# Kernel tuning notes

Measured on AMD Instinct MI355X. Metric: run time of the kernel, lower is better.

Reference implementation:

```python
import jax, jax.numpy as jnp
import numpy as np

INPUT_SIZE = 1024
HIDDEN_SIZE = 1024
BATCH = 8192


def setup_inputs() -> dict:
    key = jax.random.key(0)
    ks = jax.random.split(key, 10)
    H, I, B = HIDDEN_SIZE, INPUT_SIZE, BATCH
    s = 1.0 / np.sqrt(H)  # scale params so activations stay in sane range
    return {
        "input": jax.random.normal(ks[0], (B, I), jnp.float32),
        "hx": jax.random.normal(ks[1], (B, H), jnp.float32),
        "cx": jax.random.normal(ks[2], (B, H), jnp.float32),
        "att": jax.random.normal(ks[3], (B, I), jnp.float32),
        "weight_ih": jax.random.normal(ks[4], (4 * H, I), jnp.float32) * s,
        "weight_hh": jax.random.normal(ks[5], (4 * H, H), jnp.float32) * s,
        "bias_ih": jax.random.normal(ks[6], (4 * H,), jnp.float32),
        "bias_hh": jax.random.normal(ks[7], (4 * H,), jnp.float32),
        "weight_att": jax.random.normal(ks[8], (2 * H, I), jnp.float32) * s,
        "bias_att": jax.random.normal(ks[9], (2 * H,), jnp.float32),
    }


def reference(input, hx, cx, att, weight_ih, weight_hh, bias_ih, bias_hh,
              weight_att, bias_att):
    H = weight_hh.shape[1]
    # gates: [B, 4H]
    gates = input @ weight_ih.T + bias_ih + hx @ weight_hh.T + bias_hh
    att_gates = att @ weight_att.T + bias_att  # [B, 2H]
    ingate, forgetgate, cellgate, outgate = jnp.split(gates, 4, axis=1)
    ingate_att, attgate = jnp.split(att_gates, 2, axis=1)
    ingate = jax.nn.sigmoid(ingate)
    forgetgate = jax.nn.sigmoid(forgetgate)
    cellgate = jnp.tanh(cellgate)
    ingate_att = jax.nn.sigmoid(ingate_att)
    attgate = jnp.tanh(attgate)
    outgate = jax.nn.sigmoid(outgate)
    cy = forgetgate * cx + ingate * cellgate + ingate_att * attgate
    hy = outgate * jnp.tanh(cy)
    return (hy, cy)
```

## Files before the change

kernel.cpp:

```cpp
#include <hip/hip_runtime.h>


typedef __attribute__((ext_vector_type(8))) __bf16 bf16x8;
typedef __attribute__((ext_vector_type(8))) unsigned short ushort8;
typedef __attribute__((ext_vector_type(4))) float f32x4;
typedef __attribute__((ext_vector_type(2))) unsigned int u32x2;

#define AS1 __attribute__((address_space(1)))
#define AS3 __attribute__((address_space(3)))

__device__ __forceinline__ void gld16(const unsigned short* g, unsigned short* l) {
    __builtin_amdgcn_global_load_lds((const AS1 void*)g, (AS3 void*)l, 16, 0, 0);
}

__device__ __forceinline__ unsigned short f2bf(float f) {
    unsigned int u = __builtin_bit_cast(unsigned int, f);
    u += 0x7fffu + ((u >> 16) & 1u);
    return (unsigned short)(u >> 16);
}

__device__ __forceinline__ unsigned int cvtpk(float lo, float hi) {
    unsigned int r;
    asm("v_cvt_pk_bf16_f32 %0, %1, %2" : "=v"(r) : "v"(lo), "v"(hi));
    return r;
}

__device__ __forceinline__ float bf2f(unsigned short u) {
    unsigned int x = ((unsigned int)u) << 16;
    return __builtin_bit_cast(float, x);
}

__device__ __forceinline__ float sigmoidf_(float x) { return 1.f / (1.f + __expf(-x)); }
__device__ __forceinline__ float tanhf_(float x) {
    float e = __expf(-2.f * fabsf(x));
    float t = (1.f - e) / (1.f + e);
    return x >= 0.f ? t : -t;
}

__device__ __forceinline__ bf16x8 ldfrag(const unsigned short* p) {
    return __builtin_bit_cast(bf16x8, *(const ushort8*)p);
}

#define BARRIER __builtin_amdgcn_s_barrier()
#define LGKM_(n) asm volatile("s_waitcnt lgkmcnt(" #n ")" ::: "memory")
#define LGKM(n)  LGKM_(n)
#define FENCE    asm volatile("" ::: "memory")
#define VMW_(n) asm volatile("s_waitcnt vmcnt(" #n ")" ::: "memory")
#define VMW(n)  VMW_(n)
#define PRIO1   __builtin_amdgcn_s_setprio(1)
#define PRIO0   __builtin_amdgcn_s_setprio(0)
#define MFMA16(a, b, c) __builtin_amdgcn_mfma_f32_16x16x32_bf16(a, b, c, 0, 0, 0)

__global__ __launch_bounds__(256) void cast_all_k(
    const float* __restrict__ input, const float* __restrict__ hx,
    const float* __restrict__ att,   const float* __restrict__ w_ih,
    const float* __restrict__ w_hh,  const float* __restrict__ w_att,
    unsigned short* __restrict__ XH, unsigned short* __restrict__ ATTb,
    unsigned short* __restrict__ W4, unsigned short* __restrict__ WA)
{
    const int u = blockIdx.x * 256 + threadIdx.x;
    const float* src; unsigned short* dst; int ld, off, rel;
    if      (u < 2097152) { src = input; dst = XH;   ld = 2048; off = 0;    rel = u; }
    else if (u < 4194304) { src = hx;    dst = XH;   ld = 2048; off = 1024; rel = u - 2097152; }
    else if (u < 6291456) { src = att;   dst = ATTb; ld = 1024; off = 0;    rel = u - 4194304; }
    else if (u < 7340032) { src = w_ih;  dst = W4;   ld = 2048; off = 0;    rel = u - 6291456; }
    else if (u < 8388608) { src = w_hh;  dst = W4;   ld = 2048; off = 1024; rel = u - 7340032; }
    else                  { src = w_att; dst = WA;   ld = 1024; off = 0;    rel = u - 8388608; }

    const float4 v = *(const float4*)(src + rel * 4);
    u32x2 q;
    q[0] = cvtpk(v.x, v.y);
    q[1] = cvtpk(v.z, v.w);
    const int row = rel >> 8, c4 = rel & 255;
    *(u32x2*)(dst + row * ld + off + c4 * 4) = q;
}

__global__ __launch_bounds__(512, 2) void fused_gemm_k(
    const unsigned short* __restrict__ XH, const unsigned short* __restrict__ W4,
    const unsigned short* __restrict__ ATTb, const unsigned short* __restrict__ WA,
    const float* __restrict__ b_ih, const float* __restrict__ b_hh,
    const float* __restrict__ bias_att,
    const float* __restrict__ cx, unsigned short* __restrict__ attS,
    float* __restrict__ out)
{
    __shared__ unsigned short As[2][16384];
    __shared__ unsigned short Bs[2][16384];

    const int tid  = threadIdx.x;
    const int wave = tid >> 6, lane = tid & 63;
    const int l15 = lane & 15, quad = lane >> 4;
    const int wr = wave >> 2, wn = wave & 3;

    const int orig  = blockIdx.x;
    const int xcd   = orig & 7, local = orig >> 3;
    const int row0  = (xcd * 4 + (local & 3)) * 256;
    const int n0    = (local >> 2) * 64;

    const int rl = tid >> 3;
    const int c8 = (tid & 7) ^ (rl & 7);
    unsigned aG = (unsigned)(row0 + rl) * 2048u + (unsigned)c8 * 8u;
    unsigned bG = (unsigned)(((rl >> 4) & 3) * 1024 + n0 + (rl & 15)) * 2048u + (unsigned)c8 * 8u;
    unsigned aA = (unsigned)(row0 + rl) * 1024u + (unsigned)c8 * 8u;
    unsigned bA = (unsigned)(((rl >> 4) & 1) * 1024 + n0 + ((rl >> 5) & 1) * 16 + (rl & 15)) * 1024u
                  + (unsigned)c8 * 8u;

    auto stageA_att = [&](int buf) {
#pragma unroll
        for (int h = 0; h < 2; ++h)
#pragma unroll
            for (int p = 0; p < 2; ++p)
                gld16(ATTb + aA + (unsigned)(h * 131072 + p * 65536),
                      &As[buf][h * 8192 + (tid + p * 512) * 8]);
        aA += 64;
    };
    auto stageB_att = [&](int buf) {
#pragma unroll
        for (int h = 0; h < 2; ++h)
            gld16(WA + bA + (unsigned)(h * 32768), &Bs[buf][(h * 512 + tid) * 8]);
        bA += 64;
    };
    auto stageA_g = [&](int buf) {
#pragma unroll
        for (int h = 0; h < 2; ++h)
#pragma unroll
            for (int p = 0; p < 2; ++p)
                gld16(XH + aG + (unsigned)(h * 262144 + p * 131072),
                      &As[buf][h * 8192 + (tid + p * 512) * 8]);
        aG += 64;
    };
    auto stageB_g = [&](int buf) {
#pragma unroll
        for (int h = 0; h < 2; ++h)
#pragma unroll
            for (int p = 0; p < 2; ++p)
                gld16(W4 + bG + (unsigned)(h * 65536 + p * 32768),
                      &Bs[buf][h * 8192 + (tid + p * 512) * 8]);
        bG += 64;
    };

    const int swz0 = (quad ^ (l15 & 7)) * 8;
    const int swz1 = ((4 + quad) ^ (l15 & 7)) * 8;
    const int aro  = (wr * 128 + l15) * 64;
    const int brG  = (wn * 64 + l15) * 64;
    const int brA  = (wn * 32 + l15) * 64;

    const f32x4 z = {0.f, 0.f, 0.f, 0.f};
    const int col = n0 + wn * 16 + l15;

    {
        f32x4 acc2[8][2];
#pragma unroll
        for (int i = 0; i < 8; ++i) { acc2[i][0] = z; acc2[i][1] = z; }

        auto att_slice = [&](int buf, int sw) {
            bf16x8 aS[8], bS[2];
#pragma unroll
            for (int i = 0; i < 4; ++i) aS[i] = ldfrag(&As[buf][aro + i * 1024 + sw]);
#pragma unroll
            for (int j = 0; j < 2; ++j) bS[j] = ldfrag(&Bs[buf][brA + j * 1024 + sw]);
            FENCE;
#pragma unroll
            for (int i = 0; i < 4; ++i) aS[4 + i] = ldfrag(&As[buf][aro + (4 + i) * 1024 + sw]);
            BARRIER; LGKM(4);
            PRIO1;
#pragma unroll
            for (int i = 0; i < 4; ++i)
#pragma unroll
                for (int j = 0; j < 2; ++j)
                    acc2[i][j] = MFMA16(aS[i], bS[j], acc2[i][j]);
            LGKM(0);
#pragma unroll
            for (int i = 0; i < 4; ++i)
#pragma unroll
                for (int j = 0; j < 2; ++j)
                    acc2[4 + i][j] = MFMA16(aS[4 + i], bS[j], acc2[4 + i][j]);
            PRIO0;
            BARRIER;
        };

        stageA_att(0); stageB_att(0);
        for (int g = 0; g < 8; ++g) {
            stageA_att(1); stageB_att(1);
            VMW(6); BARRIER;
            att_slice(0, swz0);
            att_slice(0, swz1);
            if (g < 7) { stageA_att(0); stageB_att(0); VMW(6); }
            else       { VMW(0); }
            BARRIER;
            att_slice(1, swz0);
            att_slice(1, swz1);
        }

        const float ba0 = bias_att[col], ba1 = bias_att[1024 + col];
#pragma unroll
        for (int i = 0; i < 8; ++i) {
            const int lr = wr * 128 + i * 16 + quad * 4;
#pragma unroll
            for (int r = 0; r < 4; ++r) {
                float v = sigmoidf_(acc2[i][0][r] + ba0) * tanhf_(acc2[i][1][r] + ba1);
                attS[(unsigned)(row0 + lr + r) * 1024u + (unsigned)col] = f2bf(v);
            }
        }
    }

    f32x4 acc[8][4];
#pragma unroll
    for (int i = 0; i < 8; ++i)
#pragma unroll
        for (int j = 0; j < 4; ++j) acc[i][j] = z;

    auto gates_group = [&](int buf, bool iss) {
        bf16x8 aF0[4], aF1[4], aH0[4], aH1[4], bL0[2], bL1[2], bH0[2], bH1[2];
#pragma unroll
        for (int i = 0; i < 4; ++i) aF0[i] = ldfrag(&As[buf][aro + i * 1024 + swz0]);
#pragma unroll
        for (int j = 0; j < 2; ++j) bL0[j] = ldfrag(&Bs[buf][brG + j * 1024 + swz0]);
        FENCE;
#pragma unroll
        for (int i = 0; i < 4; ++i) aF1[i] = ldfrag(&As[buf][aro + i * 1024 + swz1]);
#pragma unroll
        for (int j = 0; j < 2; ++j) bL1[j] = ldfrag(&Bs[buf][brG + j * 1024 + swz1]);
        BARRIER; LGKM(6);
        PRIO1;
#pragma unroll
        for (int i = 0; i < 4; ++i)
#pragma unroll
            for (int j = 0; j < 2; ++j)
                acc[i][j] = MFMA16(aF0[i], bL0[j], acc[i][j]);
        LGKM(0);
#pragma unroll
        for (int i = 0; i < 4; ++i)
#pragma unroll
            for (int j = 0; j < 2; ++j)
                acc[i][j] = MFMA16(aF1[i], bL1[j], acc[i][j]);
        PRIO0;
        BARRIER;
#pragma unroll
        for (int j = 0; j < 2; ++j) bH0[j] = ldfrag(&Bs[buf][brG + (2 + j) * 1024 + swz0]);
        FENCE;
#pragma unroll
        for (int j = 0; j < 2; ++j) bH1[j] = ldfrag(&Bs[buf][brG + (2 + j) * 1024 + swz1]);
        BARRIER; LGKM(2);
        PRIO1;
#pragma unroll
        for (int i = 0; i < 4; ++i)
#pragma unroll
            for (int j = 0; j < 2; ++j)
                acc[i][2 + j] = MFMA16(aF0[i], bH0[j], acc[i][2 + j]);
        LGKM(0);
#pragma unroll
        for (int i = 0; i < 4; ++i)
#pragma unroll
            for (int j = 0; j < 2; ++j)
                acc[i][2 + j] = MFMA16(aF1[i], bH1[j], acc[i][2 + j]);
        PRIO0;
        BARRIER;
#pragma unroll
        for (int i = 0; i < 4; ++i) aH0[i] = ldfrag(&As[buf][aro + (4 + i) * 1024 + swz0]);
        FENCE;
#pragma unroll
        for (int i = 0; i < 4; ++i) aH1[i] = ldfrag(&As[buf][aro + (4 + i) * 1024 + swz1]);
        if (iss) stageB_g(buf);
        BARRIER; LGKM(4);
        PRIO1;
#pragma unroll
        for (int i = 0; i < 4; ++i)
#pragma unroll
            for (int j = 0; j < 2; ++j)
                acc[4 + i][2 + j] = MFMA16(aH0[i], bH0[j], acc[4 + i][2 + j]);
        LGKM(0);
#pragma unroll
        for (int i = 0; i < 4; ++i)
#pragma unroll
            for (int j = 0; j < 2; ++j)
                acc[4 + i][2 + j] = MFMA16(aH1[i], bH1[j], acc[4 + i][2 + j]);
        PRIO0;
        BARRIER;
        if (iss) stageA_g(buf);
        PRIO1;
#pragma unroll
        for (int i = 0; i < 4; ++i)
#pragma unroll
            for (int j = 0; j < 2; ++j) {
                acc[4 + i][j] = MFMA16(aH0[i], bL0[j], acc[4 + i][j]);
                acc[4 + i][j] = MFMA16(aH1[i], bL1[j], acc[4 + i][j]);
            }
        PRIO0;
    };

    stageA_g(0); stageB_g(0); stageA_g(1); stageB_g(1);
    VMW(8); BARRIER;
#pragma unroll 2
    for (int t = 0; t < 30; ++t) {
        gates_group(t & 1, true);
        VMW(8); BARRIER;
    }
    gates_group(0, false); VMW(0); BARRIER;
    gates_group(1, false);
    BARRIER;

    float* sF = (float*)(&As[0][0]);
    float* sC = (float*)(&Bs[0][0]);
    const float bi  = b_ih[col]        + b_hh[col];
    const float bff = b_ih[1024 + col] + b_hh[1024 + col];
    const float bg  = b_ih[2048 + col] + b_hh[2048 + col];
    const float bo  = b_ih[3072 + col] + b_hh[3072 + col];
    const int lcol  = wn * 16 + l15;
    const int CYOFF = 8192 * 1024;

#pragma unroll
    for (int i = 0; i < 8; ++i)
#pragma unroll
        for (int r = 0; r < 4; ++r) {
            const int lr = wr * 128 + i * 16 + quad * 4 + r;
            const int pc = lcol ^ (((lr >> 2) & 1) << 4);
            const float attv = bf2f(attS[(unsigned)(row0 + lr) * 1024u + (unsigned)col]);
            sF[lr * 64 + pc] = sigmoidf_(acc[i][1][r] + bff);
            sC[lr * 64 + pc] = sigmoidf_(acc[i][0][r] + bi) * tanhf_(acc[i][2][r] + bg)
                               + attv;
        }
    BARRIER;

    const int rr = tid >> 4;
    const int cc = (tid & 15) * 4;
#pragma unroll
    for (int p = 0; p < 8; ++p) {
        const int row = p * 32 + rr;
        const int pcc = cc ^ (((row >> 2) & 1) << 4);
        f32x4 fg4 = *(f32x4*)&sF[row * 64 + pcc];
        f32x4 cp4 = *(f32x4*)&sC[row * 64 + pcc];
        const float4 cx4 = *(const float4*)&cx[(row0 + row) * 1024 + n0 + cc];
        f32x4 cy4;
        cy4[0] = fg4[0] * cx4.x + cp4[0];
        cy4[1] = fg4[1] * cx4.y + cp4[1];
        cy4[2] = fg4[2] * cx4.z + cp4[2];
        cy4[3] = fg4[3] * cx4.w + cp4[3];
        *(f32x4*)&out[CYOFF + (row0 + row) * 1024 + n0 + cc] = cy4;
        *(f32x4*)&sF[row * 64 + pcc] = cy4;
    }
    BARRIER;

#pragma unroll
    for (int i = 0; i < 8; ++i)
#pragma unroll
        for (int r = 0; r < 4; ++r) {
            const int lr = wr * 128 + i * 16 + quad * 4 + r;
            const int pc = lcol ^ (((lr >> 2) & 1) << 4);
            sC[lr * 64 + pc] = sigmoidf_(acc[i][3][r] + bo);
        }
    BARRIER;

#pragma unroll
    for (int p = 0; p < 8; ++p) {
        const int row = p * 32 + rr;
        const int pcc = cc ^ (((row >> 2) & 1) << 4);
        f32x4 og4 = *(f32x4*)&sC[row * 64 + pcc];
        f32x4 cy4 = *(f32x4*)&sF[row * 64 + pcc];
        f32x4 hy4;
        hy4[0] = og4[0] * tanhf_(cy4[0]);
        hy4[1] = og4[1] * tanhf_(cy4[1]);
        hy4[2] = og4[2] * tanhf_(cy4[2]);
        hy4[3] = og4[3] * tanhf_(cy4[3]);
        *(f32x4*)&out[(row0 + row) * 1024 + n0 + cc] = hy4;
    }
}

extern "C" void kernel_launch(void* const* d_in, const int* in_sizes, int n_in,
                              void* d_out, int out_size, void* d_ws, size_t ws_size,
                              hipStream_t stream) {
    const float* input = (const float*)d_in[0];
    const float* hx    = (const float*)d_in[1];
    const float* cx    = (const float*)d_in[2];
    const float* att   = (const float*)d_in[3];
    const float* w_ih  = (const float*)d_in[4];
    const float* w_hh  = (const float*)d_in[5];
    const float* b_ih  = (const float*)d_in[6];
    const float* b_hh  = (const float*)d_in[7];
    const float* w_att = (const float*)d_in[8];
    const float* b_att = (const float*)d_in[9];
    float* out = (float*)d_out;

    char* ws = (char*)d_ws;
    unsigned short* XH   = (unsigned short*)(ws);
    unsigned short* ATTb = (unsigned short*)(ws + 33554432);
    unsigned short* W4   = (unsigned short*)(ws + 50331648);
    unsigned short* WA   = (unsigned short*)(ws + 67108864);
    unsigned short* attS = (unsigned short*)(ws + 71319552);

    cast_all_k<<<34816, 256, 0, stream>>>(input, hx, att, w_ih, w_hh, w_att,
                                          XH, ATTb, W4, WA);
    fused_gemm_k<<<512, 512, 0, stream>>>(XH, W4, ATTb, WA, b_ih, b_hh, b_att,
                                          cx, attS, out);
}
```

Measured before the change: 382.2 us.

## Software-pipeline LDS fragment reads across MFMA phases with fewer barriers

Both the attention GEMM loop and the gates GEMM loop are restructured so LDS fragment reads for the next k-slice or buffer are issued before the MFMAs on the current fragments, with sched_barrier fences pinning the order. Per-phase barriers are cut to two per stage and the tail iterations are folded into one loop. The goal is to hide LDS latency behind MFMA work and cut synchronisation stalls. The cost is more live fragment registers, which could lower occupancy or cause spills, and a full vmcnt(0) wait per iteration.

New measurement: 507.5 us. 1.33x slower.

```diff
diff --git a/kernel.cpp b/kernel.cpp
--- a/kernel.cpp
+++ b/kernel.cpp
@@ -44,7 +44,7 @@
 #define BARRIER __builtin_amdgcn_s_barrier()
 #define LGKM_(n) asm volatile("s_waitcnt lgkmcnt(" #n ")" ::: "memory")
 #define LGKM(n)  LGKM_(n)
-#define FENCE    asm volatile("" ::: "memory")
+#define SCHED0   __builtin_amdgcn_sched_barrier(0)
 #define VMW_(n) asm volatile("s_waitcnt vmcnt(" #n ")" ::: "memory")
 #define VMW(n)  VMW_(n)
 #define PRIO1   __builtin_amdgcn_s_setprio(1)
@@ -152,44 +152,48 @@
 #pragma unroll
         for (int i = 0; i < 8; ++i) { acc2[i][0] = z; acc2[i][1] = z; }
 
-        auto att_slice = [&](int buf, int sw) {
-            bf16x8 aS[8], bS[2];
-#pragma unroll
-            for (int i = 0; i < 4; ++i) aS[i] = ldfrag(&As[buf][aro + i * 1024 + sw]);
-#pragma unroll
-            for (int j = 0; j < 2; ++j) bS[j] = ldfrag(&Bs[buf][brA + j * 1024 + sw]);
-            FENCE;
-#pragma unroll
-            for (int i = 0; i < 4; ++i) aS[4 + i] = ldfrag(&As[buf][aro + (4 + i) * 1024 + sw]);
-            BARRIER; LGKM(4);
-            PRIO1;
-#pragma unroll
-            for (int i = 0; i < 4; ++i)
-#pragma unroll
-                for (int j = 0; j < 2; ++j)
-                    acc2[i][j] = MFMA16(aS[i], bS[j], acc2[i][j]);
-            LGKM(0);
-#pragma unroll
-            for (int i = 0; i < 4; ++i)
-#pragma unroll
-                for (int j = 0; j < 2; ++j)
-                    acc2[4 + i][j] = MFMA16(aS[4 + i], bS[j], acc2[4 + i][j]);
-            PRIO0;
+        bf16x8 aC[8], bC[2], aN[8], bN[2];
+
+#define ATT_READ(buf, sw, a, b)                                            \
+        {                                                                  \
+            _Pragma("unroll")                                              \
+            for (int i = 0; i < 8; ++i)                                    \
+                a[i] = ldfrag(&As[buf][aro + i * 1024 + (sw)]);            \
+            _Pragma("unroll")                                              \
+            for (int j = 0; j < 2; ++j)                                    \
+                b[j] = ldfrag(&Bs[buf][brA + j * 1024 + (sw)]);            \
+        }
+#define ATT_MMA(a, b)                                                      \
+        {                                                                  \
+            PRIO1;                                                         \
+            _Pragma("unroll")                                              \
+            for (int i = 0; i < 8; ++i)                                    \
+                _Pragma("unroll")                                          \
+                for (int j = 0; j < 2; ++j)                                \
+                    acc2[i][j] = MFMA16(a[i], b[j], acc2[i][j]);           \
+            PRIO0;                                                         \
+        }
+
+        stageA_att(0); stageB_att(0);
+        stageA_att(1); stageB_att(1);
+        VMW(6); BARRIER;
+        ATT_READ(0, swz0, aC, bC);
+
+        for (int t = 0; t < 16; ++t) {
+            const int buf = t & 1;
+            ATT_READ(buf, swz1, aN, bN);
+            LGKM(10); SCHED0;
+            ATT_MMA(aC, bC);
+            VMW(0); BARRIER;
+            if (t < 15) { ATT_READ(buf ^ 1, swz0, aC, bC); LGKM(10); }
+            else        { LGKM(0); }
+            SCHED0;
+            ATT_MMA(aN, bN);
             BARRIER;
-        };
-
-        stageA_att(0); stageB_att(0);
-        for (int g = 0; g < 8; ++g) {
-            stageA_att(1); stageB_att(1);
-            VMW(6); BARRIER;
-            att_slice(0, swz0);
-            att_slice(0, swz1);
-            if (g < 7) { stageA_att(0); stageB_att(0); VMW(6); }
-            else       { VMW(0); }
-            BARRIER;
-            att_slice(1, swz0);
-            att_slice(1, swz1);
-        }
+            if (t < 14) { stageA_att(buf); stageB_att(buf); }
+        }
+#undef ATT_READ
+#undef ATT_MMA
 
         const float ba0 = bias_att[col], ba1 = bias_att[1024 + col];
 #pragma unroll
@@ -209,94 +213,68 @@
 #pragma unroll
         for (int j = 0; j < 4; ++j) acc[i][j] = z;
 
-    auto gates_group = [&](int buf, bool iss) {
-        bf16x8 aF0[4], aF1[4], aH0[4], aH1[4], bL0[2], bL1[2], bH0[2], bH1[2];
-#pragma unroll
-        for (int i = 0; i < 4; ++i) aF0[i] = ldfrag(&As[buf][aro + i * 1024 + swz0]);
-#pragma unroll
-        for (int j = 0; j < 2; ++j) bL0[j] = ldfrag(&Bs[buf][brG + j * 1024 + swz0]);
-        FENCE;
-#pragma unroll
-        for (int i = 0; i < 4; ++i) aF1[i] = ldfrag(&As[buf][aro + i * 1024 + swz1]);
-#pragma unroll
-        for (int j = 0; j < 2; ++j) bL1[j] = ldfrag(&Bs[buf][brG + j * 1024 + swz1]);
-        BARRIER; LGKM(6);
-        PRIO1;
-#pragma unroll
-        for (int i = 0; i < 4; ++i)
-#pragma unroll
-            for (int j = 0; j < 2; ++j)
-                acc[i][j] = MFMA16(aF0[i], bL0[j], acc[i][j]);
-        LGKM(0);
-#pragma unroll
-        for (int i = 0; i < 4; ++i)
-#pragma unroll
-            for (int j = 0; j < 2; ++j)
-                acc[i][j] = MFMA16(aF1[i], bL1[j], acc[i][j]);
-        PRIO0;
-        BARRIER;
-#pragma unroll
-        for (int j = 0; j < 2; ++j) bH0[j] = ldfrag(&Bs[buf][brG + (2 + j) * 1024 + swz0]);
-        FENCE;
-#pragma unroll
-        for (int j = 0; j < 2; ++j) bH1[j] = ldfrag(&Bs[buf][brG + (2 + j) * 1024 + swz1]);
-        BARRIER; LGKM(2);
-        PRIO1;
-#pragma unroll
-        for (int i = 0; i < 4; ++i)
-#pragma unroll
-            for (int j = 0; j < 2; ++j)
-                acc[i][2 + j] = MFMA16(aF0[i], bH0[j], acc[i][2 + j]);
-        LGKM(0);
-#pragma unroll
-        for (int i = 0; i < 4; ++i)
-#pragma unroll
-            for (int j = 0; j < 2; ++j)
-                acc[i][2 + j] = MFMA16(aF1[i], bH1[j], acc[i][2 + j]);
-        PRIO0;
-        BARRIER;
-#pragma unroll
-        for (int i = 0; i < 4; ++i) aH0[i] = ldfrag(&As[buf][aro + (4 + i) * 1024 + swz0]);
-        FENCE;
-#pragma unroll
-        for (int i = 0; i < 4; ++i) aH1[i] = ldfrag(&As[buf][aro + (4 + i) * 1024 + swz1]);
-        if (iss) stageB_g(buf);
-        BARRIER; LGKM(4);
-        PRIO1;
-#pragma unroll
-        for (int i = 0; i < 4; ++i)
-#pragma unroll
-            for (int j = 0; j < 2; ++j)
-                acc[4 + i][2 + j] = MFMA16(aH0[i], bH0[j], acc[4 + i][2 + j]);
-        LGKM(0);
-#pragma unroll
-        for (int i = 0; i < 4; ++i)
-#pragma unroll
-            for (int j = 0; j < 2; ++j)
-                acc[4 + i][2 + j] = MFMA16(aH1[i], bH1[j], acc[4 + i][2 + j]);
-        PRIO0;
-        BARRIER;
-        if (iss) stageA_g(buf);
-        PRIO1;
-#pragma unroll
-        for (int i = 0; i < 4; ++i)
-#pragma unroll
-            for (int j = 0; j < 2; ++j) {
-                acc[4 + i][j] = MFMA16(aH0[i], bL0[j], acc[4 + i][j]);
-                acc[4 + i][j] = MFMA16(aH1[i], bL1[j], acc[4 + i][j]);
-            }
-        PRIO0;
-    };
-
-    stageA_g(0); stageB_g(0); stageA_g(1); stageB_g(1);
-    VMW(8); BARRIER;
+    {
+        bf16x8 aF0[4], aH0[4], aF1[4], aH1[4], b0[4], b1[4];
+
+        stageA_g(0); stageB_g(0);
+        stageA_g(1); stageB_g(1);
+        VMW(8); BARRIER;
+#pragma unroll
+        for (int i = 0; i < 4; ++i) aF0[i] = ldfrag(&As[0][aro + i * 1024 + swz0]);
+#pragma unroll
+        for (int j = 0; j < 4; ++j) b0[j]  = ldfrag(&Bs[0][brG + j * 1024 + swz0]);
+
 #pragma unroll 2
-    for (int t = 0; t < 30; ++t) {
-        gates_group(t & 1, true);
-        VMW(8); BARRIER;
+        for (int t = 0; t < 32; ++t) {
+            const int buf = t & 1;
+#pragma unroll
+            for (int i = 0; i < 4; ++i) aH0[i] = ldfrag(&As[buf][aro + (4 + i) * 1024 + swz0]);
+            LGKM(4); SCHED0; PRIO1;
+#pragma unroll
+            for (int i = 0; i < 4; ++i)
+#pragma unroll
+                for (int j = 0; j < 4; ++j)
+                    acc[i][j] = MFMA16(aF0[i], b0[j], acc[i][j]);
+            PRIO0;
+#pragma unroll
+            for (int i = 0; i < 4; ++i) aF1[i] = ldfrag(&As[buf][aro + i * 1024 + swz1]);
+#pragma unroll
+            for (int j = 0; j < 4; ++j) b1[j]  = ldfrag(&Bs[buf][brG + j * 1024 + swz1]);
+            LGKM(8); SCHED0; PRIO1;
+#pragma unroll
+            for (int i = 0; i < 4; ++i)
+#pragma unroll
+                for (int j = 0; j < 4; ++j)
+                    acc[4 + i][j] = MFMA16(aH0[i], b0[j], acc[4 + i][j]);
+            PRIO0;
+#pragma unroll
+            for (int i = 0; i < 4; ++i) aH1[i] = ldfrag(&As[buf][aro + (4 + i) * 1024 + swz1]);
+            LGKM(4); SCHED0; PRIO1;
+#pragma unroll
+            for (int i = 0; i < 4; ++i)
+#pragma unroll
+                for (int j = 0; j < 4; ++j)
+                    acc[i][j] = MFMA16(aF1[i], b1[j], acc[i][j]);
+            PRIO0;
+            VMW(0); BARRIER;
+            if (t < 31) {
+#pragma unroll
+                for (int i = 0; i < 4; ++i) aF0[i] = ldfrag(&As[buf ^ 1][aro + i * 1024 + swz0]);
+#pragma unroll
+                for (int j = 0; j < 4; ++j) b0[j]  = ldfrag(&Bs[buf ^ 1][brG + j * 1024 + swz0]);
+                LGKM(8);
+            } else { LGKM(0); }
+            SCHED0; PRIO1;
+#pragma unroll
+            for (int i = 0; i < 4; ++i)
+#pragma unroll
+                for (int j = 0; j < 4; ++j)
+                    acc[4 + i][j] = MFMA16(aH1[i], b1[j], acc[4 + i][j]);
+            PRIO0;
+            BARRIER;
+            if (t < 30) { stageA_g(buf); stageB_g(buf); }
+        }
     }
-    gates_group(0, false); VMW(0); BARRIER;
-    gates_group(1, false);
     BARRIER;
 
     float* sF = (float*)(&As[0][0]);
```
